# Optimization experiments

Hardware: AMD Instinct MI355X
Metric: run time of the kernel (lower is better)

Reference implementation:

```python
import jax, jax.numpy as jnp
import numpy as np

N, E, DIN, DH, DOUT, NG = 50000, 800000, 128, 128, 64, 128
EPS = 1e-5
SLOPE = 0.2  # PyG GATConv default negative_slope


def _gat(x, src, dst, W, a_s, a_d, b, heads, out_c, concat):
    n = x.shape[0]
    xp = (x @ W).reshape(n, heads, out_c)            # [N,H,C]
    e_src = (xp * a_s[None]).sum(-1)                  # [N,H]
    e_dst = (xp * a_d[None]).sum(-1)                  # [N,H]
    al = e_src[src] + e_dst[dst]                      # [E,H]
    al = jnp.where(al > 0, al, SLOPE * al)            # leaky_relu
    amax = jax.ops.segment_max(al, dst, num_segments=n)
    w = jnp.exp(al - amax[dst])                       # segment softmax (stable)
    den = jax.ops.segment_sum(w, dst, num_segments=n)
    msg = w[:, :, None] * xp[src]                     # [E,H,C]
    out = jax.ops.segment_sum(msg, dst, num_segments=n) / den[:, :, None]
    out = out.reshape(n, heads * out_c) if concat else out.mean(axis=1)
    return out + b


def _bn(h, g, be):
    m = h.mean(axis=0)
    v = h.var(axis=0)  # biased var, as in torch BN training mode
    return (h - m) / jnp.sqrt(v + EPS) * g + be


def setup_inputs() -> dict:
    key = jax.random.key(0)
    ks = jax.random.split(key, 12)
    x = jax.random.normal(ks[0], (N, DIN), dtype=jnp.float32)
    edge_index = jax.random.randint(ks[1], (2, E), 0, N, dtype=jnp.int64)
    graph_pool = jax.random.uniform(ks[2], (NG, N), dtype=jnp.float32) * (2.0 / N)
    s = 0.1
    return {
        "x": x, "edge_index": edge_index, "graph_pool": graph_pool,
        "W1": jax.random.normal(ks[3], (DIN, DH), dtype=jnp.float32) * s,
        "as1": jax.random.normal(ks[4], (1, DH), dtype=jnp.float32) * s,
        "ad1": jax.random.normal(ks[5], (1, DH), dtype=jnp.float32) * s,
        "b1": jnp.zeros((DH,), jnp.float32),
        "g1": jnp.ones((DH,), jnp.float32), "be1": jnp.zeros((DH,), jnp.float32),
        "W2": jax.random.normal(ks[6], (DH, DH), dtype=jnp.float32) * s,
        "as2": jax.random.normal(ks[7], (1, DH), dtype=jnp.float32) * s,
        "ad2": jax.random.normal(ks[8], (1, DH), dtype=jnp.float32) * s,
        "b2": jnp.zeros((DH,), jnp.float32),
        "g2": jnp.ones((DH,), jnp.float32), "be2": jnp.zeros((DH,), jnp.float32),
        "W3": jax.random.normal(ks[9], (DH, DOUT), dtype=jnp.float32) * s,
        "as3": jax.random.normal(ks[10], (1, DOUT), dtype=jnp.float32) * s,
        "ad3": jax.random.normal(ks[11], (1, DOUT), dtype=jnp.float32) * s,
        "b3": jnp.zeros((DOUT,), jnp.float32),
    }


def reference(x, edge_index, graph_pool,
              W1, as1, ad1, b1, g1, be1,
              W2, as2, ad2, b2, g2, be2,
              W3, as3, ad3, b3):
    n = x.shape[0]
    loops = jnp.arange(n, dtype=edge_index.dtype)  # PyG add_self_loops=True
    src = jnp.concatenate([edge_index[0], loops])
    dst = jnp.concatenate([edge_index[1], loops])
    h = _gat(x, src, dst, W1, as1, ad1, b1, 1, DH, True)
    h = jax.nn.relu(_bn(h, g1, be1))
    h = _gat(h, src, dst, W2, as2, ad2, b2, 1, DH, True)
    h = jax.nn.relu(_bn(h, g2, be2))
    h_nodes = _gat(h, src, dst, W3, as3, ad3, b3, 1, DOUT, False)
    h_pooled = graph_pool @ h_nodes  # sparse.mm == matmul mathematically
    return (h_pooled, h_nodes)
```

## Files before the change

### kernel.cpp

```cpp
#include <hip/hip_runtime.h>
#include <hip/hip_bf16.h>

#define DIN 128
#define DH  128
#define DOUT 64
#define NGR 128
#define EPSV 1e-5f
#define SLOPE 0.2f
#define BSH 7
#define NBMAX 512
#define BCAP 3584
#define POOLB 256
#define BNSPREAD 32

typedef __attribute__((ext_vector_type(8))) short short8;
typedef __attribute__((ext_vector_type(4))) float float4v;

__device__ __forceinline__ unsigned short f2bf(float f) {
    union { float f; unsigned int u; } v; v.f = f;
    unsigned int r = (v.u + 0x7FFFu + ((v.u >> 16) & 1u)) >> 16;
    return (unsigned short)r;
}
__device__ __forceinline__ unsigned short f2bf_f(float f) {
    return (unsigned short)((__float_as_uint(f) + 0x8000u) >> 16);
}
__device__ __forceinline__ float bf_lo(unsigned int u) { return __uint_as_float(u << 16); }
__device__ __forceinline__ float bf_hi(unsigned int u) { return __uint_as_float(u & 0xFFFF0000u); }

__device__ __forceinline__ void pack_one(const float* W, unsigned short* PW, int cout, int t) {
    int lane = t & 63;
    int ks   = (t >> 6) & 3;
    int nt   = t >> 8;
    int nn   = nt * 16 + (lane & 15);
    int k0   = ks * 32 + (lane >> 4) * 8;
    unsigned int pk[4];
#pragma unroll
    for (int p = 0; p < 4; ++p) {
        unsigned short lo = f2bf(W[(k0 + 2 * p) * cout + nn]);
        unsigned short hi = f2bf(W[(k0 + 2 * p + 1) * cout + nn]);
        pk[p] = ((unsigned int)hi << 16) | lo;
    }
    *(uint4*)&PW[(size_t)t * 8] = make_uint4(pk[0], pk[1], pk[2], pk[3]);
}

__global__ __launch_bounds__(256) void front_a_kernel(
    const int* __restrict__ ei, int* __restrict__ bucket_cnt, int2* __restrict__ binned,
    int E, int T, int nb, int binBlocks,
    const float* __restrict__ W1, unsigned short* __restrict__ PW1,
    const float* __restrict__ W2, unsigned short* __restrict__ PW2,
    const float* __restrict__ W3, unsigned short* __restrict__ PW3)
{
    if ((int)blockIdx.x >= binBlocks) {
        int t = ((int)blockIdx.x - binBlocks) * 256 + (int)threadIdx.x;
        if (t < 2048)      pack_one(W1, PW1, 128, t);
        else if (t < 4096) pack_one(W2, PW2, 128, t - 2048);
        else if (t < 5120) pack_one(W3, PW3, 64,  t - 4096);
        return;
    }
    __shared__ int hist[NBMAX], base[NBMAX], cur[NBMAX];
    for (int i = threadIdx.x; i < nb; i += 256) hist[i] = 0;
    __syncthreads();
    int start = blockIdx.x * 8192;
    int endc  = start + 8192; if (endc > T) endc = T;
    for (int e = start + threadIdx.x; e < endc; e += 256) {
        int d = (e < E) ? ei[E + e] : (e - E);
        atomicAdd(&hist[d >> BSH], 1);
    }
    __syncthreads();
    for (int i = threadIdx.x; i < nb; i += 256) {
        int h = hist[i];
        cur[i] = 0;
        if (h) base[i] = atomicAdd(&bucket_cnt[i], h);
    }
    __syncthreads();
    for (int e = start + threadIdx.x; e < endc; e += 256) {
        int s, d;
        if (e < E) { s = ei[e]; d = ei[E + e]; }
        else       { s = e - E; d = s; }
        int b = d >> BSH;
        int off = atomicAdd(&cur[b], 1);
        binned[(size_t)b * BCAP + base[b] + off] = make_int2(s, d);
    }
}

template <int COUT, int BNIN>
__device__ __forceinline__ void gemm_es_body(
    unsigned short* Xs, float* sSc, float* sSh, int row0,
    const void* __restrict__ Xv, const unsigned short* __restrict__ PW,
    const float* __restrict__ a_s, const float* __restrict__ a_d,
    const float* __restrict__ bnsum, const float* __restrict__ g,
    const float* __restrict__ be, float invn,
    unsigned short* __restrict__ XPB, float* __restrict__ e_src, float* __restrict__ e_dst, int n)
{
    constexpr int NT = COUT / 16;
    int tid = threadIdx.x;

    if constexpr (BNIN) {
        if (tid < 128) {
            float s = 0.f, q = 0.f;
#pragma unroll 4
            for (int k = 0; k < BNSPREAD; ++k) {
                s += bnsum[k * 256 + tid];
                q += bnsum[k * 256 + 128 + tid];
            }
            float mean = s * invn;
            float var  = q * invn - mean * mean;
            float sc   = g[tid] * rsqrtf(var + EPSV);
            sSc[tid] = sc;
            sSh[tid] = be[tid] - mean * sc;
        }
        __syncthreads();
        const unsigned short* H = (const unsigned short*)Xv;
        for (int i = tid; i < 64 * 16; i += 256) {
            int r  = i >> 4;
            int c8 = (i & 15) * 8;
            uint4 u = make_uint4(0, 0, 0, 0);
            if (row0 + r < n) u = *(const uint4*)&H[(size_t)(row0 + r) * 128 + c8];
            unsigned int uu[4] = {u.x, u.y, u.z, u.w};
            unsigned int out[4];
#pragma unroll
            for (int p = 0; p < 4; ++p) {
                int c = c8 + 2 * p;
                float a  = fmaxf(bf_lo(uu[p]) * sSc[c] + sSh[c], 0.f);
                float bq = fmaxf(bf_hi(uu[p]) * sSc[c + 1] + sSh[c + 1], 0.f);
                out[p] = ((unsigned int)f2bf_f(bq) << 16) | f2bf_f(a);
            }
            *(uint4*)&Xs[r * 136 + c8] = make_uint4(out[0], out[1], out[2], out[3]);
        }
    } else {
        const float* X = (const float*)Xv;
        for (int i = tid; i < 64 * 32; i += 256) {
            int r  = i >> 5;
            int k4 = (i & 31) * 4;
            float4 v = make_float4(0.f, 0.f, 0.f, 0.f);
            if (row0 + r < n) v = *(const float4*)&X[(size_t)(row0 + r) * 128 + k4];
            uint2 pk;
            pk.x = ((unsigned int)f2bf_f(v.y) << 16) | f2bf_f(v.x);
            pk.y = ((unsigned int)f2bf_f(v.w) << 16) | f2bf_f(v.z);
            *(uint2*)&Xs[r * 136 + k4] = pk;
        }
    }
    __syncthreads();

    int wv   = tid >> 6;
    int lane = tid & 63;
    int m0   = wv * 16;
    int cl   = lane & 15;
    int q    = lane >> 4;

    float4v acc[NT] = {};
#pragma unroll
    for (int ks = 0; ks < 4; ++ks) {
        short8 af = *(const short8*)&Xs[(m0 + cl) * 136 + ks * 32 + q * 8];
#pragma unroll
        for (int nt = 0; nt < NT; ++nt) {
            short8 bf = *(const short8*)&PW[(size_t)((nt * 4 + ks) * 64 + lane) * 8];
            acc[nt] = __builtin_amdgcn_mfma_f32_16x16x32_bf16(af, bf, acc[nt], 0, 0, 0);
        }
    }

    float asv[NT], adv[NT];
#pragma unroll
    for (int nt = 0; nt < NT; ++nt) {
        asv[nt] = a_s[nt * 16 + cl];
        adv[nt] = a_d[nt * 16 + cl];
    }
#pragma unroll
    for (int reg = 0; reg < 4; ++reg) {
        int m = row0 + m0 + q * 4 + reg;
        if (m >= n) continue;
        float ps = 0.f, pd = 0.f;
        size_t base = (size_t)m * COUT;
#pragma unroll
        for (int nt = 0; nt < NT; ++nt) {
            float v = acc[nt][reg];
            XPB[base + nt * 16 + cl] = f2bf_f(v);
            ps += v * asv[nt];
            pd += v * adv[nt];
        }
        ps += __shfl_xor(ps, 1); pd += __shfl_xor(pd, 1);
        ps += __shfl_xor(ps, 2); pd += __shfl_xor(pd, 2);
        ps += __shfl_xor(ps, 4); pd += __shfl_xor(pd, 4);
        ps += __shfl_xor(ps, 8); pd += __shfl_xor(pd, 8);
        if (cl == 0) {
            e_src[m] = ps;
            e_dst[m] = pd;
        }
    }
}

template <int COUT, int BNIN>
__global__ __launch_bounds__(256) void gemm_es_kernel(
    const void* __restrict__ Xv, const unsigned short* __restrict__ PW,
    const float* __restrict__ a_s, const float* __restrict__ a_d,
    const float* __restrict__ bnsum, const float* __restrict__ g,
    const float* __restrict__ be, float invn,
    unsigned short* __restrict__ XPB, float* __restrict__ e_src, float* __restrict__ e_dst, int n)
{
    __shared__ unsigned short Xs[64 * 136];
    __shared__ float sSc[128], sSh[128];
    gemm_es_body<COUT, BNIN>(Xs, sSc, sSh, blockIdx.x * 64,
                             Xv, PW, a_s, a_d, bnsum, g, be, invn, XPB, e_src, e_dst, n);
}

__global__ __launch_bounds__(256) void front_b_kernel(
    const int2* __restrict__ binned, const int* __restrict__ bucket_cnt,
    int* __restrict__ row_ptr, int* __restrict__ col_src, int n, int T, int nbcsr,
    const float* __restrict__ X, const unsigned short* __restrict__ PW,
    const float* __restrict__ a_s, const float* __restrict__ a_d,
    unsigned short* __restrict__ XPB, float* __restrict__ e_src, float* __restrict__ e_dst)
{
    __shared__ __align__(16) char smraw[64 * 136 * 2];
    int tid = threadIdx.x;

    if ((int)blockIdx.x < nbcsr) {
        int* cnt = (int*)smraw;
        int* rnk = cnt + 128;
        int* rp  = rnk + 128;
        int* sc  = rp + 128;
        int* red = sc + 128;
        int b = blockIdx.x;
        int node0 = b << BSH;
        const int2* bin = &binned[(size_t)b * BCAP];
        int nb_edges = bucket_cnt[b];

        int part = 0;
        for (int i = tid; i < b; i += 256) part += bucket_cnt[i];
        red[tid] = part;
        if (tid < 128) cnt[tid] = 0;
        __syncthreads();
#pragma unroll
        for (int s2 = 128; s2 > 0; s2 >>= 1) {
            if (tid < s2) red[tid] += red[tid + s2];
            __syncthreads();
        }
        int lo = red[0];

        for (int i = tid; i < nb_edges; i += 256)
            atomicAdd(&cnt[bin[i].y - node0], 1);
        __syncthreads();
        if (tid < 128) sc[tid] = cnt[tid];
        __syncthreads();
        for (int d2 = 1; d2 < 128; d2 <<= 1) {
            int t = 0;
            if (tid < 128 && tid >= d2) t = sc[tid - d2];
            __syncthreads();
            if (tid < 128) sc[tid] += t;
            __syncthreads();
        }
        if (tid < 128) {
            int excl = sc[tid] - cnt[tid];
            int r = lo + excl;
            rp[tid] = r;
            rnk[tid] = 0;
            int node = node0 + tid;
            if (node < n) row_ptr[node] = r;
        }
        if (b == 0 && tid == 0) row_ptr[n] = T;
        __syncthreads();
        for (int i = tid; i < nb_edges; i += 256) {
            int2 e = bin[i];
            int local = e.y - node0;
            int r = atomicAdd(&rnk[local], 1);
            col_src[rp[local] + r] = e.x;
        }
    } else {
        unsigned short* Xs = (unsigned short*)smraw;
        gemm_es_body<128, 0>(Xs, nullptr, nullptr, ((int)blockIdx.x - nbcsr) * 64,
                             X, PW, a_s, a_d, nullptr, nullptr, nullptr, 0.f,
                             XPB, e_src, e_dst, n);
    }
}

template <int COUT, int OUTBF, int BNOUT>
__global__ __launch_bounds__(256) void gat_aggregate_kernel(
    const unsigned short* __restrict__ XPB, const float* __restrict__ e_src,
    const float* __restrict__ e_dst, const int* __restrict__ row_ptr,
    const int* __restrict__ col_src, const float* __restrict__ bias,
    void* __restrict__ OUT, unsigned short* __restrict__ HNT,
    float* __restrict__ bnsumS, int n)
{
    __shared__ float bnsh[BNOUT ? 512 : 1];
    int wave = threadIdx.x >> 6;
    int lane = threadIdx.x & 63;
    int d = blockIdx.x * 4 + wave;
    bool act = (d < n);
    if (!BNOUT && !act) return;

    int start = 0, end = 0;
    float ed = 0.f;
    if (act) {
        start = row_ptr[d];
        end   = row_ptr[d + 1];
        ed    = e_dst[d];
    }

    float denl = 0.f;
    float2 acc2 = make_float2(0.f, 0.f);
    float acc1 = 0.f;
    const unsigned int* xpu = (const unsigned int*)XPB;

    for (int base = start; base < end; base += 64) {
        int t = base + lane;
        int s_l = 0; float w_l = 0.f;
        if (t < end) {
            s_l = col_src[t];
            float a = e_src[s_l] + ed;
            a = (a > 0.f) ? a : SLOPE * a;
            w_l = __expf(a);
        }
        denl += w_l;
        int cnt = end - base; if (cnt > 64) cnt = 64;
        unsigned int w_u = __float_as_uint(w_l);

        int j = 0;
        for (; j + 7 < cnt; j += 8) {
            int ss[8]; float ww[8];
#pragma unroll
            for (int p = 0; p < 8; ++p) {
                ss[p] = __builtin_amdgcn_readlane(s_l, j + p);
                ww[p] = __uint_as_float(__builtin_amdgcn_readlane(w_u, j + p));
            }
            if (COUT == 128) {
                unsigned int us[8];
#pragma unroll
                for (int p = 0; p < 8; ++p)
                    us[p] = (xpu + ((size_t)(unsigned)ss[p] << 6))[lane];
#pragma unroll
                for (int p = 0; p < 8; ++p) {
                    acc2.x += ww[p] * bf_lo(us[p]);
                    acc2.y += ww[p] * bf_hi(us[p]);
                }
            } else {
                float xs[8];
#pragma unroll
                for (int p = 0; p < 8; ++p)
                    xs[p] = __uint_as_float((unsigned int)(XPB + ((size_t)(unsigned)ss[p] << 6))[lane] << 16);
#pragma unroll
                for (int p = 0; p < 8; ++p) acc1 += ww[p] * xs[p];
            }
        }
        for (; j + 3 < cnt; j += 4) {
            int ss[4]; float ww[4];
#pragma unroll
            for (int p = 0; p < 4; ++p) {
                ss[p] = __builtin_amdgcn_readlane(s_l, j + p);
                ww[p] = __uint_as_float(__builtin_amdgcn_readlane(w_u, j + p));
            }
            if (COUT == 128) {
                unsigned int us[4];
#pragma unroll
                for (int p = 0; p < 4; ++p)
                    us[p] = (xpu + ((size_t)(unsigned)ss[p] << 6))[lane];
#pragma unroll
                for (int p = 0; p < 4; ++p) {
                    acc2.x += ww[p] * bf_lo(us[p]);
                    acc2.y += ww[p] * bf_hi(us[p]);
                }
            } else {
#pragma unroll
                for (int p = 0; p < 4; ++p) {
                    float xv = __uint_as_float((unsigned int)(XPB + ((size_t)(unsigned)ss[p] << 6))[lane] << 16);
                    acc1 += ww[p] * xv;
                }
            }
        }
        for (; j < cnt; ++j) {
            int   s = __builtin_amdgcn_readlane(s_l, j);
            float w = __uint_as_float(__builtin_amdgcn_readlane(w_u, j));
            if (COUT == 128) {
                unsigned int u = (xpu + ((size_t)(unsigned)s << 6))[lane];
                acc2.x += w * bf_lo(u);
                acc2.y += w * bf_hi(u);
            } else {
                acc1 += w * __uint_as_float((unsigned int)(XPB + ((size_t)(unsigned)s << 6))[lane] << 16);
            }
        }
    }

#pragma unroll
    for (int off = 1; off < 64; off <<= 1) denl += __shfl_xor(denl, off);
    float inv = 1.f / denl;

    if (COUT == 128) {
        float ox = 0.f, oy = 0.f;
        if (act) {
            ox = acc2.x * inv + bias[2 * lane + 0];
            oy = acc2.y * inv + bias[2 * lane + 1];
            if (OUTBF) {
                unsigned int o = ((unsigned int)f2bf_f(oy) << 16) | f2bf_f(ox);
                ((unsigned int*)OUT)[(size_t)d * 64 + lane] = o;
            } else {
                ((float2*)OUT)[(size_t)d * 64 + lane] = make_float2(ox, oy);
            }
        }
        if (BNOUT) {
            bnsh[wave * 128 + 2 * lane]     = ox;
            bnsh[wave * 128 + 2 * lane + 1] = oy;
            __syncthreads();
            if (wave == 0) {
                float s0 = 0.f, q0 = 0.f, s1 = 0.f, q1 = 0.f;
#pragma unroll
                for (int k = 0; k < 4; ++k) {
                    float v0 = bnsh[k * 128 + 2 * lane];
                    float v1 = bnsh[k * 128 + 2 * lane + 1];
                    s0 += v0; q0 += v0 * v0;
                    s1 += v1; q1 += v1 * v1;
                }
                float* dstb = &bnsumS[(blockIdx.x & (BNSPREAD - 1)) * 256];
                atomicAdd(&dstb[2 * lane],           s0);
                atomicAdd(&dstb[2 * lane + 1],       s1);
                atomicAdd(&dstb[128 + 2 * lane],     q0);
                atomicAdd(&dstb[128 + 2 * lane + 1], q1);
            }
        }
    } else {
        float o = acc1 * inv + bias[lane];
        ((float*)OUT)[(size_t)d * COUT + lane] = o;
        HNT[(size_t)lane * n + d] = f2bf_f(o);
    }
}

__global__ __launch_bounds__(256) void pool_mfma_kernel(
    const float* __restrict__ GP, const unsigned short* __restrict__ HNT,
    float* __restrict__ partial, int n, int nchunk)
{
    __shared__ unsigned short gp_s[128 * 136];
    __shared__ unsigned short ht_s[64 * 136];
    int tid = threadIdx.x;
    int wv = tid >> 6, lane = tid & 63, cl = lane & 15, q = lane >> 4;

    float4v acc[4][2] = {};

    for (int blk = blockIdx.x; blk < nchunk; blk += gridDim.x) {
        int k0 = blk * 128;

        for (int i = tid; i < 128 * 8; i += 256) {
            int r  = i >> 3;
            int kk = (i & 7) * 16;
            int gk = k0 + kk;
            const float* src = &GP[(size_t)r * n + gk];
            unsigned int pk[8];
#pragma unroll
            for (int q2 = 0; q2 < 4; ++q2) {
                float4 v = make_float4(0.f, 0.f, 0.f, 0.f);
                if (gk + q2 * 4 < n) v = *(const float4*)&src[q2 * 4];
                pk[2 * q2 + 0] = ((unsigned int)f2bf_f(v.y) << 16) | f2bf_f(v.x);
                pk[2 * q2 + 1] = ((unsigned int)f2bf_f(v.w) << 16) | f2bf_f(v.z);
            }
            *(uint4*)&gp_s[r * 136 + kk]     = make_uint4(pk[0], pk[1], pk[2], pk[3]);
            *(uint4*)&gp_s[r * 136 + kk + 8] = make_uint4(pk[4], pk[5], pk[6], pk[7]);
        }
        for (int i = tid; i < 64 * 16; i += 256) {
            int r  = i >> 4;
            int kk = (i & 15) * 8;
            int gk = k0 + kk;
            uint4 v = make_uint4(0, 0, 0, 0);
            if (gk < n) v = *(const uint4*)&HNT[(size_t)r * n + gk];
            *(uint4*)&ht_s[r * 136 + kk] = v;
        }
        __syncthreads();

#pragma unroll
        for (int ks = 0; ks < 4; ++ks) {
            short8 bfr[2];
#pragma unroll
            for (int j = 0; j < 2; ++j)
                bfr[j] = *(const short8*)&gp_s[((wv * 2 + j) * 16 + cl) * 136 + ks * 32 + q * 8];
#pragma unroll
            for (int mt = 0; mt < 4; ++mt) {
                short8 af = *(const short8*)&ht_s[(mt * 16 + cl) * 136 + ks * 32 + q * 8];
#pragma unroll
                for (int j = 0; j < 2; ++j)
                    acc[mt][j] = __builtin_amdgcn_mfma_f32_16x16x32_bf16(af, bfr[j], acc[mt][j], 0, 0, 0);
            }
        }
        __syncthreads();
    }

    float* po = &partial[(size_t)blockIdx.x * (NGR * DOUT)];
#pragma unroll
    for (int mt = 0; mt < 4; ++mt) {
#pragma unroll
        for (int j = 0; j < 2; ++j) {
            int g = (wv * 2 + j) * 16 + cl;
            int c = mt * 16 + q * 4;
            *(float4*)&po[g * 64 + c] =
                make_float4(acc[mt][j][0], acc[mt][j][1], acc[mt][j][2], acc[mt][j][3]);
        }
    }
}

__global__ __launch_bounds__(256) void pool_reduce_kernel(
    const float* __restrict__ partial, float* __restrict__ OUT, int nblk)
{
    int i = blockIdx.x * 256 + threadIdx.x;
    float s0 = 0.f, s1 = 0.f, s2 = 0.f, s3 = 0.f;
    int p = 0;
    for (; p + 3 < nblk; p += 4) {
        s0 += partial[(size_t)(p + 0) * (NGR * DOUT) + i];
        s1 += partial[(size_t)(p + 1) * (NGR * DOUT) + i];
        s2 += partial[(size_t)(p + 2) * (NGR * DOUT) + i];
        s3 += partial[(size_t)(p + 3) * (NGR * DOUT) + i];
    }
    for (; p < nblk; ++p) s0 += partial[(size_t)p * (NGR * DOUT) + i];
    OUT[i] = (s0 + s1) + (s2 + s3);
}

extern "C" void kernel_launch(void* const* d_in, const int* in_sizes, int n_in,
                              void* d_out, int out_size, void* d_ws, size_t ws_size,
                              hipStream_t stream) {
    const float* x   = (const float*)d_in[0];
    const int*   ei  = (const int*)d_in[1];
    const float* gp  = (const float*)d_in[2];
    const float* W1  = (const float*)d_in[3];
    const float* as1 = (const float*)d_in[4];
    const float* ad1 = (const float*)d_in[5];
    const float* b1  = (const float*)d_in[6];
    const float* g1  = (const float*)d_in[7];
    const float* be1 = (const float*)d_in[8];
    const float* W2  = (const float*)d_in[9];
    const float* as2 = (const float*)d_in[10];
    const float* ad2 = (const float*)d_in[11];
    const float* b2  = (const float*)d_in[12];
    const float* g2  = (const float*)d_in[13];
    const float* be2 = (const float*)d_in[14];
    const float* W3  = (const float*)d_in[15];
    const float* as3 = (const float*)d_in[16];
    const float* ad3 = (const float*)d_in[17];
    const float* b3  = (const float*)d_in[18];

    const int N = in_sizes[0] / DIN;
    const int E = in_sizes[1] / 2;
    const int T = E + N;
    const int NB = (N + 127) >> BSH;

    char* ws = (char*)d_ws;
    auto take = [&](size_t bytes) {
        char* p = ws;
        ws += (bytes + 511) & ~(size_t)511;
        return p;
    };
    unsigned short* xpb = (unsigned short*)take((size_t)N * 128 * 2);
    unsigned short* h   = (unsigned short*)take((size_t)N * 128 * 2);
    unsigned short* hnt = (unsigned short*)take((size_t)64 * N * 2);
    float* pool_s  = (float*)take((size_t)POOLB * NGR * DOUT * 4);
    float* esd     = (float*)take((size_t)2 * N * 4);
    float* e_src   = esd;
    float* e_dst   = esd + N;
    int*   row_ptr = (int*)take((size_t)(N + 1) * 4);
    int*   col_src = (int*)take((size_t)T * 4);
    int2*  binned  = (int2*)take((size_t)NB * BCAP * 8);
    int*   zero_rgn   = (int*)take((size_t)(NBMAX + 1 + 2 * BNSPREAD * 256) * 4);
    int*   bucket_cnt = zero_rgn;
    float* bnsum1     = (float*)(zero_rgn + NBMAX + 1);
    float* bnsum2     = bnsum1 + BNSPREAD * 256;
    unsigned short* pw1 = (unsigned short*)take((size_t)128 * 128 * 2);
    unsigned short* pw2 = (unsigned short*)take((size_t)128 * 128 * 2);
    unsigned short* pw3 = (unsigned short*)take((size_t)128 * 64 * 2);

    float* outp = (float*)d_out;
    float* hn   = outp + NGR * DOUT;

    hipMemsetAsync(zero_rgn, 0, (size_t)(NBMAX + 1 + 2 * BNSPREAD * 256) * 4, stream);

    const int binBlocks = (T + 8191) / 8192;
    front_a_kernel<<<binBlocks + 20, 256, 0, stream>>>(ei, bucket_cnt, binned, E, T, NB, binBlocks,
                                                       W1, pw1, W2, pw2, W3, pw3);

    const int gx = (N + 63) / 64;
    const float invn = 1.f / N;

    front_b_kernel<<<NB + gx, 256, 0, stream>>>(binned, bucket_cnt, row_ptr, col_src, N, T, NB,
                                                x, pw1, as1, ad1, xpb, e_src, e_dst);

    gat_aggregate_kernel<128, 1, 1><<<(N + 3) / 4, 256, 0, stream>>>(
        xpb, e_src, e_dst, row_ptr, col_src, b1, h, nullptr, bnsum1, N);

    gemm_es_kernel<128, 1><<<gx, 256, 0, stream>>>(h, pw2, as2, ad2,
        bnsum1, g1, be1, invn, xpb, e_src, e_dst, N);
    gat_aggregate_kernel<128, 1, 1><<<(N + 3) / 4, 256, 0, stream>>>(
        xpb, e_src, e_dst, row_ptr, col_src, b2, h, nullptr, bnsum2, N);

    gemm_es_kernel<64, 1><<<gx, 256, 0, stream>>>(h, pw3, as3, ad3,
        bnsum2, g2, be2, invn, xpb, e_src, e_dst, N);
    gat_aggregate_kernel<64, 0, 0><<<(N + 3) / 4, 256, 0, stream>>>(
        xpb, e_src, e_dst, row_ptr, col_src, b3, hn, hnt, nullptr, N);

    const int nchunk = (N + 127) / 128;
    const int pb = nchunk < POOLB ? nchunk : POOLB;
    pool_mfma_kernel<<<pb, 256, 0, stream>>>(gp, hnt, pool_s, N, nchunk);
    pool_reduce_kernel<<<(NGR * DOUT + 255) / 256, 256, 0, stream>>>(pool_s, outp, pb);
}
```

Baseline: 346.0 us.

## Gather neighbor rows with 16-byte loads across lane groups in GAT aggregation

Reorganizes the aggregate kernel so each wave splits into lane groups that each fetch a whole neighbor row with uint4 (16-byte) loads, processing several edges in parallel instead of one edge per wave-wide 4-byte load. Per-lane partial sums over 8 channels are then reduced across groups with xor shuffles, and only group 0 writes vectorized outputs. This aims to cut the number of gather load instructions and raise bytes per memory request on the irregular neighbor reads. In exchange it adds a cross-lane reduction at the end, uses more registers, and makes most lanes idle during the stores.

```diff
diff --git a/kernel.cpp b/kernel.cpp
--- a/kernel.cpp
+++ b/kernel.cpp
@@ -281,8 +281,14 @@
     float* __restrict__ bnsumS, int n)
 {
     __shared__ float bnsh[BNOUT ? 512 : 1];
+    constexpr int GSH  = (COUT == 128) ? 4 : 3;
+    constexpr int STEP = 64 >> GSH;
+    constexpr int RSH  = (COUT == 128) ? 7 : 6;
+
     int wave = threadIdx.x >> 6;
     int lane = threadIdx.x & 63;
+    int g    = lane >> GSH;
+    int cl   = lane & ((1 << GSH) - 1);
     int d = blockIdx.x * 4 + wave;
     bool act = (d < n);
     if (!BNOUT && !act) return;
@@ -296,9 +302,7 @@
     }
 
     float denl = 0.f;
-    float2 acc2 = make_float2(0.f, 0.f);
-    float acc1 = 0.f;
-    const unsigned int* xpu = (const unsigned int*)XPB;
+    float acc8[8] = {};
 
     for (int base = start; base < end; base += 64) {
         int t = base + lane;
@@ -311,92 +315,93 @@
         }
         denl += w_l;
         int cnt = end - base; if (cnt > 64) cnt = 64;
-        unsigned int w_u = __float_as_uint(w_l);
 
         int j = 0;
-        for (; j + 7 < cnt; j += 8) {
-            int ss[8]; float ww[8];
-#pragma unroll
-            for (int p = 0; p < 8; ++p) {
-                ss[p] = __builtin_amdgcn_readlane(s_l, j + p);
-                ww[p] = __uint_as_float(__builtin_amdgcn_readlane(w_u, j + p));
-            }
+        for (; j + 16 <= cnt; j += 16) {
+            int   r0 = __shfl(s_l, j + g);
+            int   r1 = __shfl(s_l, j + STEP + g);
+            float w0 = __shfl(w_l, j + g);
+            float w1 = __shfl(w_l, j + STEP + g);
+            uint4 u0 = ((const uint4*)(XPB + ((size_t)(unsigned)r0 << RSH)))[cl];
+            uint4 u1 = ((const uint4*)(XPB + ((size_t)(unsigned)r1 << RSH)))[cl];
+            int   r2, r3; float w2, w3; uint4 u2, u3;
             if (COUT == 128) {
-                unsigned int us[8];
-#pragma unroll
-                for (int p = 0; p < 8; ++p)
-                    us[p] = (xpu + ((size_t)(unsigned)ss[p] << 6))[lane];
-#pragma unroll
-                for (int p = 0; p < 8; ++p) {
-                    acc2.x += ww[p] * bf_lo(us[p]);
-                    acc2.y += ww[p] * bf_hi(us[p]);
+                r2 = __shfl(s_l, j + 2 * STEP + g);
+                r3 = __shfl(s_l, j + 3 * STEP + g);
+                w2 = __shfl(w_l, j + 2 * STEP + g);
+                w3 = __shfl(w_l, j + 3 * STEP + g);
+                u2 = ((const uint4*)(XPB + ((size_t)(unsigned)r2 << RSH)))[cl];
+                u3 = ((const uint4*)(XPB + ((size_t)(unsigned)r3 << RSH)))[cl];
+            }
+            unsigned int a0[4] = {u0.x, u0.y, u0.z, u0.w};
+            unsigned int a1[4] = {u1.x, u1.y, u1.z, u1.w};
+#pragma unroll
+            for (int p = 0; p < 4; ++p) {
+                acc8[2 * p]     += w0 * bf_lo(a0[p]);
+                acc8[2 * p + 1] += w0 * bf_hi(a0[p]);
+                acc8[2 * p]     += w1 * bf_lo(a1[p]);
+                acc8[2 * p + 1] += w1 * bf_hi(a1[p]);
+            }
+            if (COUT == 128) {
+                unsigned int a2[4] = {u2.x, u2.y, u2.z, u2.w};
+                unsigned int a3[4] = {u3.x, u3.y, u3.z, u3.w};
+#pragma unroll
+                for (int p = 0; p < 4; ++p) {
+                    acc8[2 * p]     += w2 * bf_lo(a2[p]);
+                    acc8[2 * p + 1] += w2 * bf_hi(a2[p]);
+                    acc8[2 * p]     += w3 * bf_lo(a3[p]);
+                    acc8[2 * p + 1] += w3 * bf_hi(a3[p]);
                 }
-            } else {
-                float xs[8];
-#pragma unroll
-                for (int p = 0; p < 8; ++p)
-                    xs[p] = __uint_as_float((unsigned int)(XPB + ((size_t)(unsigned)ss[p] << 6))[lane] << 16);
-#pragma unroll
-                for (int p = 0; p < 8; ++p) acc1 += ww[p] * xs[p];
-            }
-        }
-        for (; j + 3 < cnt; j += 4) {
-            int ss[4]; float ww[4];
+            }
+        }
+        for (; j < cnt; j += STEP) {
+            int   r = __shfl(s_l, j + g);
+            float w = __shfl(w_l, j + g);
+            uint4 u = ((const uint4*)(XPB + ((size_t)(unsigned)r << RSH)))[cl];
+            unsigned int au[4] = {u.x, u.y, u.z, u.w};
 #pragma unroll
             for (int p = 0; p < 4; ++p) {
-                ss[p] = __builtin_amdgcn_readlane(s_l, j + p);
-                ww[p] = __uint_as_float(__builtin_amdgcn_readlane(w_u, j + p));
-            }
-            if (COUT == 128) {
-                unsigned int us[4];
-#pragma unroll
-                for (int p = 0; p < 4; ++p)
-                    us[p] = (xpu + ((size_t)(unsigned)ss[p] << 6))[lane];
-#pragma unroll
-                for (int p = 0; p < 4; ++p) {
-                    acc2.x += ww[p] * bf_lo(us[p]);
-                    acc2.y += ww[p] * bf_hi(us[p]);
-                }
-            } else {
-#pragma unroll
-                for (int p = 0; p < 4; ++p) {
-                    float xv = __uint_as_float((unsigned int)(XPB + ((size_t)(unsigned)ss[p] << 6))[lane] << 16);
-                    acc1 += ww[p] * xv;
-                }
-            }
-        }
-        for (; j < cnt; ++j) {
-            int   s = __builtin_amdgcn_readlane(s_l, j);
-            float w = __uint_as_float(__builtin_amdgcn_readlane(w_u, j));
-            if (COUT == 128) {
-                unsigned int u = (xpu + ((size_t)(unsigned)s << 6))[lane];
-                acc2.x += w * bf_lo(u);
-                acc2.y += w * bf_hi(u);
-            } else {
-                acc1 += w * __uint_as_float((unsigned int)(XPB + ((size_t)(unsigned)s << 6))[lane] << 16);
-            }
-        }
-    }
+                acc8[2 * p]     += w * bf_lo(au[p]);
+                acc8[2 * p + 1] += w * bf_hi(au[p]);
+            }
+        }
+    }
+
+#pragma unroll
+    for (int off = (1 << GSH); off < 64; off <<= 1)
+#pragma unroll
+        for (int k = 0; k < 8; ++k) acc8[k] += __shfl_xor(acc8[k], off);
 
 #pragma unroll
     for (int off = 1; off < 64; off <<= 1) denl += __shfl_xor(denl, off);
     float inv = 1.f / denl;
 
+    float ox[8];
+#pragma unroll
+    for (int k = 0; k < 8; ++k) ox[k] = 0.f;
+    if (act) {
+#pragma unroll
+        for (int k = 0; k < 8; ++k) ox[k] = acc8[k] * inv + bias[cl * 8 + k];
+    }
+
     if (COUT == 128) {
-        float ox = 0.f, oy = 0.f;
-        if (act) {
-            ox = acc2.x * inv + bias[2 * lane + 0];
-            oy = acc2.y * inv + bias[2 * lane + 1];
+        if (act && g == 0) {
             if (OUTBF) {
-                unsigned int o = ((unsigned int)f2bf_f(oy) << 16) | f2bf_f(ox);
-                ((unsigned int*)OUT)[(size_t)d * 64 + lane] = o;
+                unsigned int o0 = ((unsigned int)f2bf_f(ox[1]) << 16) | f2bf_f(ox[0]);
+                unsigned int o1 = ((unsigned int)f2bf_f(ox[3]) << 16) | f2bf_f(ox[2]);
+                unsigned int o2 = ((unsigned int)f2bf_f(ox[5]) << 16) | f2bf_f(ox[4]);
+                unsigned int o3 = ((unsigned int)f2bf_f(ox[7]) << 16) | f2bf_f(ox[6]);
+                ((uint4*)OUT)[(size_t)d * 16 + cl] = make_uint4(o0, o1, o2, o3);
             } else {
-                ((float2*)OUT)[(size_t)d * 64 + lane] = make_float2(ox, oy);
+                ((float4*)OUT)[(size_t)d * 32 + cl * 2]     = make_float4(ox[0], ox[1], ox[2], ox[3]);
+                ((float4*)OUT)[(size_t)d * 32 + cl * 2 + 1] = make_float4(ox[4], ox[5], ox[6], ox[7]);
             }
         }
         if (BNOUT) {
-            bnsh[wave * 128 + 2 * lane]     = ox;
-            bnsh[wave * 128 + 2 * lane + 1] = oy;
+            if (g == 0) {
+#pragma unroll
+                for (int k = 0; k < 8; ++k) bnsh[wave * 128 + cl * 8 + k] = ox[k];
+            }
             __syncthreads();
             if (wave == 0) {
                 float s0 = 0.f, q0 = 0.f, s1 = 0.f, q1 = 0.f;
@@ -415,9 +420,13 @@
             }
         }
     } else {
-        float o = acc1 * inv + bias[lane];
-        ((float*)OUT)[(size_t)d * COUT + lane] = o;
-        HNT[(size_t)lane * n + d] = f2bf_f(o);
+        if (act && g == 0) {
+            ((float4*)OUT)[(size_t)d * 16 + cl * 2]     = make_float4(ox[0], ox[1], ox[2], ox[3]);
+            ((float4*)OUT)[(size_t)d * 16 + cl * 2 + 1] = make_float4(ox[4], ox[5], ox[6], ox[7]);
+#pragma unroll
+            for (int k = 0; k < 8; ++k)
+                HNT[(size_t)(cl * 8 + k) * n + d] = f2bf_f(ox[k]);
+        }
     }
 }
 
```

Result: no change. 344.1 us (-0.6%).
